# Kernel tuning notes

Hardware: AMD Instinct MI355X
Metric: run time of the kernel (lower is better)

The kernel has to match this reference:

```python
import jax, jax.numpy as jnp
import numpy as np

B, T, IN_DIM, LATENT, NUM_TOKENS = 8, 2048, 1024, 256, 4096


def setup_inputs() -> dict:
    key = jax.random.key(0)
    k1, k2, k3 = jax.random.split(key, 3)
    x = jax.random.normal(k1, (B, T, IN_DIM), dtype=jnp.float32)
    # Linear projection params (Kaiming-ish scale)
    W = jax.random.normal(k2, (IN_DIM, LATENT), dtype=jnp.float32) / np.sqrt(IN_DIM)
    b = jnp.zeros((LATENT,), dtype=jnp.float32)
    # Codebook (nn.Embedding with xavier_uniform init ~ small normal here)
    codebook = jax.random.normal(k3, (NUM_TOKENS, LATENT), dtype=jnp.float32) * 0.05
    return {"x": x, "W": W, "b": b, "codebook": codebook}


def reference(x, W, b, codebook):
    # normalization='none' -> identity; projection: Linear(in_dim, latent_dim)
    h = jnp.einsum("btd,de->bte", x, W) + b              # [B,T,latent]
    flat = h.reshape(-1, h.shape[-1])                     # [N,latent]
    # cdist + argmin: squared distance gives identical argmin as euclidean
    # d2[n,k] = |flat[n]|^2 - 2 flat@cb^T + |cb[k]|^2
    d2 = (jnp.sum(flat * flat, axis=-1, keepdims=True)
          - 2.0 * (flat @ codebook.T)
          + jnp.sum(codebook * codebook, axis=-1))        # [N,num_tokens]
    indices = jnp.argmin(d2, axis=-1)                     # [N]
    codes = codebook[indices].reshape(h.shape)            # gather -> [B,T,latent]
    idx = indices.reshape(x.shape[:-1] + (1,))            # [B,T,1]
    return codes, idx
```

## Files before the change

kernel.cpp:

```cpp
#include <hip/hip_runtime.h>

#define NROWS   16384
#define INDIM   1024
#define KDIM    256
#define NCODES  4096
#define G_ROWS  32
#define V_ROWS  64
#define NSTEP   128

#define VBUF    32768

#define MG_ROWS 64
#define MG_KC   64
#define MG_NCH  (INDIM / MG_KC)
#define XP(p)   ((p) * 8192)
#define WP(p)   (24576 + (p) * 32768)
#define MG_LDS  122880

typedef float f32x4 __attribute__((ext_vector_type(4)));
typedef int   i32x4 __attribute__((ext_vector_type(4)));
typedef short short8 __attribute__((ext_vector_type(8)));
typedef unsigned short u16x8 __attribute__((ext_vector_type(8)));
typedef unsigned short u16x4 __attribute__((ext_vector_type(4)));

__device__ inline unsigned short f2bf(float f) {
    unsigned u = __builtin_bit_cast(unsigned, f);
    u = (u + 0x7fffu + ((u >> 16) & 1u)) >> 16;
    return (unsigned short)u;
}
__device__ inline float bf2f(unsigned short h) {
    unsigned u = ((unsigned)h) << 16;
    return __builtin_bit_cast(float, u);
}
__device__ inline f32x4 mfma16(u16x8 a, u16x8 b, f32x4 c) {
    return __builtin_amdgcn_mfma_f32_16x16x32_bf16(
        __builtin_bit_cast(short8, a), __builtin_bit_cast(short8, b), c, 0, 0, 0);
}

__global__ __launch_bounds__(256) void wprep_kernel(const float* __restrict__ W,
                                                    unsigned short* __restrict__ wt_hi,
                                                    unsigned short* __restrict__ wt_md,
                                                    unsigned short* __restrict__ wt_lo) {
    const int t = threadIdx.x;
    const int k = blockIdx.x * 4 + (t >> 6);
    const int c0 = (t & 63) * 4;
    f32x4 v = *(const f32x4*)(W + (size_t)k * KDIM + c0);
    #pragma unroll
    for (int i = 0; i < 4; ++i) {
        const unsigned short h = f2bf(v[i]);
        const float r1 = v[i] - bf2f(h);
        const unsigned short m = f2bf(r1);
        const unsigned short lo = f2bf(r1 - bf2f(m));
        wt_hi[(size_t)(c0 + i) * INDIM + k] = h;
        wt_md[(size_t)(c0 + i) * INDIM + k] = m;
        wt_lo[(size_t)(c0 + i) * INDIM + k] = lo;
    }
}

__global__ __launch_bounds__(256, 1) void gemm_mfma_kernel(const float* __restrict__ x,
                                                           const unsigned short* __restrict__ wt_hi,
                                                           const unsigned short* __restrict__ wt_md,
                                                           const unsigned short* __restrict__ wt_lo,
                                                           const float* __restrict__ bvec,
                                                           float* __restrict__ hbuf) {
    __shared__ __align__(16) char lds[MG_LDS];

    const int t  = threadIdx.x;
    const int w  = t >> 6;
    const int l  = t & 63;
    const int nl = l & 15;
    const int g  = l >> 4;
    const size_t n0 = (size_t)blockIdx.x * MG_ROWS;
    const int lb = l * 16;

    f32x4 acc[4][4];
    #pragma unroll
    for (int a = 0; a < 4; ++a)
        #pragma unroll
        for (int b = 0; b < 4; ++b) acc[a][b] = (f32x4){0.f, 0.f, 0.f, 0.f};

    for (int kc = 0; kc < MG_NCH; ++kc) {
        f32x4 xa[2], xb[2];
        #pragma unroll
        for (int c = 0; c < 2; ++c) {
            const int idx = w * 2 + c;
            const int sX = idx >> 2, rsX = idx & 3;
            const float* p = x + (n0 + rsX * 16 + nl) * INDIM + kc * MG_KC + sX * 32 + g * 8;
            xa[c] = *(const f32x4*)(p);
            xb[c] = *(const f32x4*)(p + 4);
        }
        u16x8 wh[8], wm[8], wl[8];
        #pragma unroll
        for (int ci = 0; ci < 4; ++ci)
            #pragma unroll
            for (int sW = 0; sW < 2; ++sW) {
                const int q = ci * 2 + sW;
                const size_t off = (size_t)((w * 4 + ci) * 16 + nl) * INDIM
                                 + kc * MG_KC + sW * 32 + g * 8;
                wh[q] = *(const u16x8*)(wt_hi + off);
                wm[q] = *(const u16x8*)(wt_md + off);
                wl[q] = *(const u16x8*)(wt_lo + off);
            }
        __syncthreads();

        #pragma unroll
        for (int c = 0; c < 2; ++c) {
            const int idx = w * 2 + c;
            const int sX = idx >> 2, rsX = idx & 3;
            u16x8 xh, xm, xl;
            #pragma unroll
            for (int e = 0; e < 4; ++e) {
                const float a0 = xa[c][e], a1 = xb[c][e];
                const unsigned short h0 = f2bf(a0);
                const float r10 = a0 - bf2f(h0);
                const unsigned short m0 = f2bf(r10);
                const unsigned short l0 = f2bf(r10 - bf2f(m0));
                const unsigned short h1 = f2bf(a1);
                const float r11 = a1 - bf2f(h1);
                const unsigned short m1 = f2bf(r11);
                const unsigned short l1 = f2bf(r11 - bf2f(m1));
                xh[e] = h0; xh[4+e] = h1;
                xm[e] = m0; xm[4+e] = m1;
                xl[e] = l0; xl[4+e] = l1;
            }
            const int base = (sX * 4 + rsX) * 1024 + lb;
            *(u16x8*)(lds + XP(0) + base) = xh;
            *(u16x8*)(lds + XP(1) + base) = xm;
            *(u16x8*)(lds + XP(2) + base) = xl;
        }
        #pragma unroll
        for (int ci = 0; ci < 4; ++ci)
            #pragma unroll
            for (int sW = 0; sW < 2; ++sW) {
                const int q = ci * 2 + sW;
                const int base = (sW * 16 + w * 4 + ci) * 1024 + lb;
                *(u16x8*)(lds + WP(0) + base) = wh[q];
                *(u16x8*)(lds + WP(1) + base) = wm[q];
                *(u16x8*)(lds + WP(2) + base) = wl[q];
            }
        __syncthreads();

        #pragma unroll
        for (int s = 0; s < 2; ++s) {
            u16x8 bh[4], bm[4], bl[4], ah[4], am[4], al[4];
            #pragma unroll
            for (int rs = 0; rs < 4; ++rs) {
                const int base = (s * 4 + rs) * 1024 + lb;
                bh[rs] = *(const u16x8*)(lds + XP(0) + base);
                bm[rs] = *(const u16x8*)(lds + XP(1) + base);
                bl[rs] = *(const u16x8*)(lds + XP(2) + base);
            }
            #pragma unroll
            for (int ct = 0; ct < 4; ++ct) {
                const int base = (s * 16 + w * 4 + ct) * 1024 + lb;
                ah[ct] = *(const u16x8*)(lds + WP(0) + base);
                am[ct] = *(const u16x8*)(lds + WP(1) + base);
                al[ct] = *(const u16x8*)(lds + WP(2) + base);
            }
            #pragma unroll
            for (int ct = 0; ct < 4; ++ct)
                #pragma unroll
                for (int rs = 0; rs < 4; ++rs) {
                    acc[ct][rs] = mfma16(ah[ct], bh[rs], acc[ct][rs]);
                    acc[ct][rs] = mfma16(ah[ct], bm[rs], acc[ct][rs]);
                    acc[ct][rs] = mfma16(am[ct], bh[rs], acc[ct][rs]);
                    acc[ct][rs] = mfma16(ah[ct], bl[rs], acc[ct][rs]);
                    acc[ct][rs] = mfma16(al[ct], bh[rs], acc[ct][rs]);
                    acc[ct][rs] = mfma16(am[ct], bm[rs], acc[ct][rs]);
                }
        }
    }

    #pragma unroll
    for (int ct = 0; ct < 4; ++ct) {
        float bv[4];
        #pragma unroll
        for (int r = 0; r < 4; ++r) bv[r] = bvec[w * 64 + ct * 16 + g * 4 + r];
        #pragma unroll
        for (int rs = 0; rs < 4; ++rs) {
            const size_t row = n0 + rs * 16 + nl;
            #pragma unroll
            for (int r = 0; r < 4; ++r)
                hbuf[row * KDIM + w * 64 + ct * 16 + g * 4 + r] = acc[ct][rs][r] + bv[r];
        }
    }
}

__global__ __launch_bounds__(256, 2) void gemm_fb_kernel(const float* __restrict__ x,
                                                         const float* __restrict__ W,
                                                         const float* __restrict__ bvec,
                                                         float* __restrict__ hbuf) {
    const int t  = threadIdx.x;
    const int cg = t & 15;
    const int rg = t >> 4;
    const size_t n0 = (size_t)blockIdx.x * G_ROWS;
    const int c0 = cg * 16;

    float acc[2][16];
    #pragma unroll
    for (int j = 0; j < 2; ++j)
        #pragma unroll
        for (int cc = 0; cc < 16; ++cc) acc[j][cc] = 0.f;

    for (int k4 = 0; k4 < INDIM / 4; ++k4) {
        const int k = k4 * 4;
        f32x4 xv[2];
        #pragma unroll
        for (int j = 0; j < 2; ++j)
            xv[j] = *(const f32x4*)(x + (n0 + rg + 16 * j) * INDIM + k);
        f32x4 wv[4][4];
        #pragma unroll
        for (int kk = 0; kk < 4; ++kk)
            #pragma unroll
            for (int q = 0; q < 4; ++q)
                wv[kk][q] = *(const f32x4*)(W + (size_t)(k + kk) * KDIM + c0 + 4 * q);
        #pragma unroll
        for (int j = 0; j < 2; ++j)
            #pragma unroll
            for (int kk = 0; kk < 4; ++kk) {
                const float xs = xv[j][kk];
                #pragma unroll
                for (int q = 0; q < 4; ++q)
                    #pragma unroll
                    for (int e = 0; e < 4; ++e)
                        acc[j][4*q+e] = fmaf(xs, wv[kk][q][e], acc[j][4*q+e]);
            }
    }
    #pragma unroll
    for (int j = 0; j < 2; ++j) {
        float* dst = hbuf + (n0 + rg + 16 * j) * KDIM + c0;
        #pragma unroll
        for (int q = 0; q < 4; ++q) {
            f32x4 v;
            #pragma unroll
            for (int e = 0; e < 4; ++e) v[e] = acc[j][4*q+e] + bvec[c0 + 4*q + e];
            *(f32x4*)(dst + 4*q) = v;
        }
    }
}

__global__ __launch_bounds__(256) void prep_kernel(const float* __restrict__ cb,
                                                   float* __restrict__ cnorm,
                                                   unsigned short* __restrict__ cb_hi,
                                                   unsigned short* __restrict__ cb_lo,
                                                   int do_split) {
    const int c    = blockIdx.x * 4 + (threadIdx.x >> 6);
    const int lane = threadIdx.x & 63;
    f32x4 v = ((const f32x4*)(cb + (size_t)c * KDIM))[lane];
    if (do_split) {
        u16x4 h4, l4;
        #pragma unroll
        for (int j = 0; j < 4; ++j) {
            unsigned short h = f2bf(v[j]);
            h4[j] = h;
            l4[j] = f2bf(v[j] - bf2f(h));
        }
        *(u16x4*)(cb_hi + (size_t)c * KDIM + lane * 4) = h4;
        *(u16x4*)(cb_lo + (size_t)c * KDIM + lane * 4) = l4;
    }
    float s = v[0]*v[0] + v[1]*v[1] + v[2]*v[2] + v[3]*v[3];
    #pragma unroll
    for (int off = 1; off < 64; off <<= 1) s += __shfl_xor(s, off);
    if (lane == 0) cnorm[c] = s;
}

template<int PRE>
__global__ __launch_bounds__(256) void vq_partial_kernel(
    const float* __restrict__ hbuf,
    const float* __restrict__ cb,
    const float* __restrict__ cnorm,
    const unsigned short* __restrict__ cb_hi,
    const unsigned short* __restrict__ cb_lo,
    int* __restrict__ recs)
{
    __shared__ __align__(16) char lds[2 * VBUF];

    const int t  = threadIdx.x;
    const int w  = t >> 6;
    const int l  = t & 63;
    const int nl = l & 15;
    const int g  = l >> 4;
    const int lb = l * 16;
    const int bid  = blockIdx.x;
    const int half = bid & 1;
    const int S0   = half * 64;
    const size_t n0 = (size_t)(bid >> 1) * V_ROWS;
    const int row = w * 16 + nl;
    const float* hrow = hbuf + (n0 + row) * KDIM;

    u16x8 bhi[8], bmid[8];
    #pragma unroll
    for (int s = 0; s < 8; ++s) {
        f32x4 a = *(const f32x4*)(hrow + s * 32 + g * 8);
        f32x4 b = *(const f32x4*)(hrow + s * 32 + g * 8 + 4);
        u16x8 uh, um;
        #pragma unroll
        for (int jj = 0; jj < 4; ++jj) {
            unsigned short h0 = f2bf(a[jj]); uh[jj]   = h0; um[jj]   = f2bf(a[jj] - bf2f(h0));
            unsigned short h1 = f2bf(b[jj]); uh[4+jj] = h1; um[4+jj] = f2bf(b[jj] - bf2f(h1));
        }
        bhi[s] = uh; bmid[s] = um;
    }

    float v1 = 3.4e38f, v2 = 3.4e38f;
    int   i1 = 0, i2 = 0;

    u16x8 rh[2][2], rl[2][2];

    #pragma unroll
    for (int t2 = 0; t2 < 2; ++t2)
        #pragma unroll
        for (int sv = 0; sv < 2; ++sv) {
            const int sst = w * 2 + sv;
            const int code = S0 * 32 + t2 * 16 + nl;
            if (PRE) {
                const size_t off = (size_t)code * KDIM + (sst * 4 + g) * 8;
                rh[t2][sv] = *(const u16x8*)(cb_hi + off);
                rl[t2][sv] = *(const u16x8*)(cb_lo + off);
            } else {
                const float* p = cb + (size_t)code * KDIM + (sst * 4 + g) * 8;
                f32x4 a = *(const f32x4*)(p);
                f32x4 b = *(const f32x4*)(p + 4);
                u16x8 uh, ul;
                #pragma unroll
                for (int jj = 0; jj < 4; ++jj) {
                    unsigned short h0 = f2bf(a[jj]); uh[jj]   = h0; ul[jj]   = f2bf(a[jj] - bf2f(h0));
                    unsigned short h1 = f2bf(b[jj]); uh[4+jj] = h1; ul[4+jj] = f2bf(b[jj] - bf2f(h1));
                }
                rh[t2][sv] = uh; rl[t2][sv] = ul;
            }
        }
    #pragma unroll
    for (int t2 = 0; t2 < 2; ++t2)
        #pragma unroll
        for (int sv = 0; sv < 2; ++sv) {
            const int base = (t2 * 8 + w * 2 + sv) * 1024 + lb;
            *(u16x8*)(lds + base) = rh[t2][sv];
            *(u16x8*)(lds + 16384 + base) = rl[t2][sv];
        }
    __syncthreads();

    for (int S = S0; S < S0 + 64; ++S) {
        const int b = S & 1;
        if (S + 1 < S0 + 64) {
            #pragma unroll
            for (int t2 = 0; t2 < 2; ++t2)
                #pragma unroll
                for (int sv = 0; sv < 2; ++sv) {
                    const int sst = w * 2 + sv;
                    const int code = (S + 1) * 32 + t2 * 16 + nl;
                    if (PRE) {
                        const size_t off = (size_t)code * KDIM + (sst * 4 + g) * 8;
                        rh[t2][sv] = *(const u16x8*)(cb_hi + off);
                        rl[t2][sv] = *(const u16x8*)(cb_lo + off);
                    } else {
                        const float* p = cb + (size_t)code * KDIM + (sst * 4 + g) * 8;
                        f32x4 a = *(const f32x4*)(p);
                        f32x4 bb = *(const f32x4*)(p + 4);
                        u16x8 uh, ul;
                        #pragma unroll
                        for (int jj = 0; jj < 4; ++jj) {
                            unsigned short h0 = f2bf(a[jj]);  uh[jj]   = h0; ul[jj]   = f2bf(a[jj] - bf2f(h0));
                            unsigned short h1 = f2bf(bb[jj]); uh[4+jj] = h1; ul[4+jj] = f2bf(bb[jj] - bf2f(h1));
                        }
                        rh[t2][sv] = uh; rl[t2][sv] = ul;
                    }
                }
        }
        f32x4 cn0 = *(const f32x4*)(cnorm + S * 32 + g * 4);
        f32x4 cn1 = *(const f32x4*)(cnorm + S * 32 + 16 + g * 4);
        {
            const char* buf = lds + b * VBUF;
            #pragma unroll
            for (int t2 = 0; t2 < 2; ++t2) {
                f32x4 acc = {0.f, 0.f, 0.f, 0.f};
                #pragma unroll
                for (int s = 0; s < 8; ++s) {
                    const int base = (t2 * 8 + s) * 1024 + lb;
                    u16x8 ahi = *(const u16x8*)(buf + base);
                    u16x8 alo = *(const u16x8*)(buf + 16384 + base);
                    acc = mfma16(ahi, bhi[s],  acc);
                    acc = mfma16(ahi, bmid[s], acc);
                    acc = mfma16(alo, bhi[s],  acc);
                }
                const f32x4 cn = t2 ? cn1 : cn0;
                #pragma unroll
                for (int r = 0; r < 4; ++r) {
                    const float d2 = cn[r] - 2.0f * acc[r];
                    const int c = S * 32 + t2 * 16 + g * 4 + r;
                    if (d2 < v1)      { v2 = v1; i2 = i1; v1 = d2; i1 = c; }
                    else if (d2 < v2) { v2 = d2; i2 = c; }
                }
            }
        }
        __syncthreads();
        if (S + 1 < S0 + 64) {
            char* nbuf = lds + (b ^ 1) * VBUF;
            #pragma unroll
            for (int t2 = 0; t2 < 2; ++t2)
                #pragma unroll
                for (int sv = 0; sv < 2; ++sv) {
                    const int base = (t2 * 8 + w * 2 + sv) * 1024 + lb;
                    *(u16x8*)(nbuf + base) = rh[t2][sv];
                    *(u16x8*)(nbuf + 16384 + base) = rl[t2][sv];
                }
        }
        __syncthreads();
    }

    #pragma unroll
    for (int off = 16; off <= 32; off <<= 1) {
        float ov1 = __shfl_xor(v1, off); int oi1 = __shfl_xor(i1, off);
        float ov2 = __shfl_xor(v2, off); int oi2 = __shfl_xor(i2, off);
        if (ov1 < v1 || (ov1 == v1 && oi1 < i1)) {
            float tv = v1; int ti = i1; v1 = ov1; i1 = oi1; ov1 = tv; oi1 = ti;
            tv = v2; ti = i2; v2 = ov2; i2 = oi2; ov2 = tv; oi2 = ti;
        }
        if (ov1 < v2 || (ov1 == v2 && oi1 < i2)) { v2 = ov1; i2 = oi1; }
    }

    if (g == 0) {
        i32x4 rec;
        rec[0] = __builtin_bit_cast(int, v1); rec[1] = i1;
        rec[2] = __builtin_bit_cast(int, v2); rec[3] = i2;
        *(i32x4*)(recs + (((n0 + row) * 2) + half) * 4) = rec;
    }
}

__global__ __launch_bounds__(256) void vq_merge_kernel(
    float* __restrict__ hbuf,
    const float* __restrict__ cb,
    const float* __restrict__ cnorm,
    const int* __restrict__ recs,
    float* __restrict__ idx_out)
{
    const int t  = threadIdx.x;
    const int w  = t >> 6;
    const int l  = t & 63;
    const int nl = l & 15;
    const int g  = l >> 4;
    const size_t n0 = (size_t)blockIdx.x * V_ROWS;
    const int row = w * 16 + nl;
    float* hrow = hbuf + (n0 + row) * KDIM;

    const size_t rb = ((n0 + row) * 2) * 4;
    i32x4 r0 = *(const i32x4*)(recs + rb);
    i32x4 r1 = *(const i32x4*)(recs + rb + 4);
    float v1 = __builtin_bit_cast(float, r0[0]); int i1 = r0[1];
    float v2 = __builtin_bit_cast(float, r0[2]); int i2 = r0[3];
    {
        float ov1 = __builtin_bit_cast(float, r1[0]); int oi1 = r1[1];
        float ov2 = __builtin_bit_cast(float, r1[2]); int oi2 = r1[3];
        if (ov1 < v1 || (ov1 == v1 && oi1 < i1)) {
            float tv = v1; int ti = i1; v1 = ov1; i1 = oi1; ov1 = tv; oi1 = ti;
            tv = v2; ti = i2; v2 = ov2; i2 = oi2; ov2 = tv; oi2 = ti;
        }
        if (ov1 < v2 || (ov1 == v2 && oi1 < i2)) { v2 = ov1; i2 = oi1; }
    }

    i1 = (i1 < 0) ? 0 : (i1 > NCODES - 1 ? NCODES - 1 : i1);
    i2 = (i2 < 0) ? 0 : (i2 > NCODES - 1 ? NCODES - 1 : i2);

    const float* cp1 = cb + (size_t)i1 * KDIM;
    const float* cp2 = cb + (size_t)i2 * KDIM;
    float da = 0.f, db = 0.f;
    #pragma unroll
    for (int s = 0; s < 8; ++s) {
        f32x4 h0 = *(const f32x4*)(hrow + s * 32 + g * 8);
        f32x4 h1 = *(const f32x4*)(hrow + s * 32 + g * 8 + 4);
        f32x4 a1 = *(const f32x4*)(cp1 + s * 32 + g * 8);
        f32x4 b1 = *(const f32x4*)(cp1 + s * 32 + g * 8 + 4);
        f32x4 a2 = *(const f32x4*)(cp2 + s * 32 + g * 8);
        f32x4 b2 = *(const f32x4*)(cp2 + s * 32 + g * 8 + 4);
        #pragma unroll
        for (int jj = 0; jj < 4; ++jj) {
            da = fmaf(a1[jj], h0[jj], da); da = fmaf(b1[jj], h1[jj], da);
            db = fmaf(a2[jj], h0[jj], db); db = fmaf(b2[jj], h1[jj], db);
        }
    }
    da += __shfl_xor(da, 16); da += __shfl_xor(da, 32);
    db += __shfl_xor(db, 16); db += __shfl_xor(db, 32);
    const float d2a = cnorm[i1] - 2.f * da;
    const float d2b = cnorm[i2] - 2.f * db;
    const int win = (d2a < d2b || (d2a == d2b && i1 < i2)) ? i1 : i2;

    const float* cw = cb + (size_t)win * KDIM;
    #pragma unroll
    for (int s = 0; s < 8; ++s) {
        *(f32x4*)(hrow + s * 32 + g * 8)     = *(const f32x4*)(cw + s * 32 + g * 8);
        *(f32x4*)(hrow + s * 32 + g * 8 + 4) = *(const f32x4*)(cw + s * 32 + g * 8 + 4);
    }
    if (g == 0) idx_out[n0 + row] = (float)win;
}

template<int PRE>
__global__ __launch_bounds__(256) void vq_kernel(
    float* __restrict__ hbuf,
    const float* __restrict__ cb,
    const float* __restrict__ cnorm,
    const unsigned short* __restrict__ cb_hi,
    const unsigned short* __restrict__ cb_lo,
    float* __restrict__ idx_out)
{
    __shared__ __align__(16) char lds[2 * VBUF];

    const int t  = threadIdx.x;
    const int w  = t >> 6;
    const int l  = t & 63;
    const int nl = l & 15;
    const int g  = l >> 4;
    const int lb = l * 16;
    const size_t n0 = (size_t)blockIdx.x * V_ROWS;
    const int row = w * 16 + nl;
    float* hrow = hbuf + (n0 + row) * KDIM;

    u16x8 bhi[8], bmid[8];
    #pragma unroll
    for (int s = 0; s < 8; ++s) {
        f32x4 a = *(const f32x4*)(hrow + s * 32 + g * 8);
        f32x4 b = *(const f32x4*)(hrow + s * 32 + g * 8 + 4);
        u16x8 uh, um;
        #pragma unroll
        for (int jj = 0; jj < 4; ++jj) {
            unsigned short h0 = f2bf(a[jj]); uh[jj]   = h0; um[jj]   = f2bf(a[jj] - bf2f(h0));
            unsigned short h1 = f2bf(b[jj]); uh[4+jj] = h1; um[4+jj] = f2bf(b[jj] - bf2f(h1));
        }
        bhi[s] = uh; bmid[s] = um;
    }

    float v1 = 3.4e38f, v2 = 3.4e38f;
    int   i1 = 0, i2 = 0;

    u16x8 rh[2][2], rl[2][2];

    #pragma unroll
    for (int t2 = 0; t2 < 2; ++t2)
        #pragma unroll
        for (int sv = 0; sv < 2; ++sv) {
            const int sst = w * 2 + sv;
            if (PRE) {
                const size_t off = (size_t)(t2 * 16 + nl) * KDIM + (sst * 4 + g) * 8;
                rh[t2][sv] = *(const u16x8*)(cb_hi + off);
                rl[t2][sv] = *(const u16x8*)(cb_lo + off);
            } else {
                const float* p = cb + (size_t)(t2 * 16 + nl) * KDIM + (sst * 4 + g) * 8;
                f32x4 a = *(const f32x4*)(p);
                f32x4 b = *(const f32x4*)(p + 4);
                u16x8 uh, ul;
                #pragma unroll
                for (int jj = 0; jj < 4; ++jj) {
                    unsigned short h0 = f2bf(a[jj]); uh[jj]   = h0; ul[jj]   = f2bf(a[jj] - bf2f(h0));
                    unsigned short h1 = f2bf(b[jj]); uh[4+jj] = h1; ul[4+jj] = f2bf(b[jj] - bf2f(h1));
                }
                rh[t2][sv] = uh; rl[t2][sv] = ul;
            }
        }
    #pragma unroll
    for (int t2 = 0; t2 < 2; ++t2)
        #pragma unroll
        for (int sv = 0; sv < 2; ++sv) {
            const int base = (t2 * 8 + w * 2 + sv) * 1024 + lb;
            *(u16x8*)(lds + base) = rh[t2][sv];
            *(u16x8*)(lds + 16384 + base) = rl[t2][sv];
        }
    __syncthreads();

    for (int S = 0; S < NSTEP; ++S) {
        const int b = S & 1;
        if (S + 1 < NSTEP) {
            #pragma unroll
            for (int t2 = 0; t2 < 2; ++t2)
                #pragma unroll
                for (int sv = 0; sv < 2; ++sv) {
                    const int sst = w * 2 + sv;
                    const int code = (S + 1) * 32 + t2 * 16 + nl;
                    if (PRE) {
                        const size_t off = (size_t)code * KDIM + (sst * 4 + g) * 8;
                        rh[t2][sv] = *(const u16x8*)(cb_hi + off);
                        rl[t2][sv] = *(const u16x8*)(cb_lo + off);
                    } else {
                        const float* p = cb + (size_t)code * KDIM + (sst * 4 + g) * 8;
                        f32x4 a = *(const f32x4*)(p);
                        f32x4 bb = *(const f32x4*)(p + 4);
                        u16x8 uh, ul;
                        #pragma unroll
                        for (int jj = 0; jj < 4; ++jj) {
                            unsigned short h0 = f2bf(a[jj]);  uh[jj]   = h0; ul[jj]   = f2bf(a[jj] - bf2f(h0));
                            unsigned short h1 = f2bf(bb[jj]); uh[4+jj] = h1; ul[4+jj] = f2bf(bb[jj] - bf2f(h1));
                        }
                        rh[t2][sv] = uh; rl[t2][sv] = ul;
                    }
                }
        }
        f32x4 cn0 = *(const f32x4*)(cnorm + S * 32 + g * 4);
        f32x4 cn1 = *(const f32x4*)(cnorm + S * 32 + 16 + g * 4);
        {
            const char* buf = lds + b * VBUF;
            #pragma unroll
            for (int t2 = 0; t2 < 2; ++t2) {
                f32x4 acc = {0.f, 0.f, 0.f, 0.f};
                #pragma unroll
                for (int s = 0; s < 8; ++s) {
                    const int base = (t2 * 8 + s) * 1024 + lb;
                    u16x8 ahi = *(const u16x8*)(buf + base);
                    u16x8 alo = *(const u16x8*)(buf + 16384 + base);
                    acc = mfma16(ahi, bhi[s],  acc);
                    acc = mfma16(ahi, bmid[s], acc);
                    acc = mfma16(alo, bhi[s],  acc);
                }
                const f32x4 cn = t2 ? cn1 : cn0;
                #pragma unroll
                for (int r = 0; r < 4; ++r) {
                    const float d2 = cn[r] - 2.0f * acc[r];
                    const int c = S * 32 + t2 * 16 + g * 4 + r;
                    if (d2 < v1)      { v2 = v1; i2 = i1; v1 = d2; i1 = c; }
                    else if (d2 < v2) { v2 = d2; i2 = c; }
                }
            }
        }
        __syncthreads();
        if (S + 1 < NSTEP) {
            char* nbuf = lds + (b ^ 1) * VBUF;
            #pragma unroll
            for (int t2 = 0; t2 < 2; ++t2)
                #pragma unroll
                for (int sv = 0; sv < 2; ++sv) {
                    const int base = (t2 * 8 + w * 2 + sv) * 1024 + lb;
                    *(u16x8*)(nbuf + base) = rh[t2][sv];
                    *(u16x8*)(nbuf + 16384 + base) = rl[t2][sv];
                }
        }
        __syncthreads();
    }

    #pragma unroll
    for (int off = 16; off <= 32; off <<= 1) {
        float ov1 = __shfl_xor(v1, off); int oi1 = __shfl_xor(i1, off);
        float ov2 = __shfl_xor(v2, off); int oi2 = __shfl_xor(i2, off);
        if (ov1 < v1 || (ov1 == v1 && oi1 < i1)) {
            float tv = v1; int ti = i1; v1 = ov1; i1 = oi1; ov1 = tv; oi1 = ti;
            tv = v2; ti = i2; v2 = ov2; i2 = oi2; ov2 = tv; oi2 = ti;
        }
        if (ov1 < v2 || (ov1 == v2 && oi1 < i2)) { v2 = ov1; i2 = oi1; }
    }

    i1 = (i1 < 0) ? 0 : (i1 > NCODES - 1 ? NCODES - 1 : i1);
    i2 = (i2 < 0) ? 0 : (i2 > NCODES - 1 ? NCODES - 1 : i2);

    const float* cp1 = cb + (size_t)i1 * KDIM;
    const float* cp2 = cb + (size_t)i2 * KDIM;
    float da = 0.f, db = 0.f;
    #pragma unroll
    for (int s = 0; s < 8; ++s) {
        f32x4 h0 = *(const f32x4*)(hrow + s * 32 + g * 8);
        f32x4 h1 = *(const f32x4*)(hrow + s * 32 + g * 8 + 4);
        f32x4 a1 = *(const f32x4*)(cp1 + s * 32 + g * 8);
        f32x4 b1 = *(const f32x4*)(cp1 + s * 32 + g * 8 + 4);
        f32x4 a2 = *(const f32x4*)(cp2 + s * 32 + g * 8);
        f32x4 b2 = *(const f32x4*)(cp2 + s * 32 + g * 8 + 4);
        #pragma unroll
        for (int jj = 0; jj < 4; ++jj) {
            da = fmaf(a1[jj], h0[jj], da); da = fmaf(b1[jj], h1[jj], da);
            db = fmaf(a2[jj], h0[jj], db); db = fmaf(b2[jj], h1[jj], db);
        }
    }
    da += __shfl_xor(da, 16); da += __shfl_xor(da, 32);
    db += __shfl_xor(db, 16); db += __shfl_xor(db, 32);
    const float d2a = cnorm[i1] - 2.f * da;
    const float d2b = cnorm[i2] - 2.f * db;
    const int win = (d2a < d2b || (d2a == d2b && i1 < i2)) ? i1 : i2;

    const float* cw = cb + (size_t)win * KDIM;
    #pragma unroll
    for (int s = 0; s < 8; ++s) {
        *(f32x4*)(hrow + s * 32 + g * 8)     = *(const f32x4*)(cw + s * 32 + g * 8);
        *(f32x4*)(hrow + s * 32 + g * 8 + 4) = *(const f32x4*)(cw + s * 32 + g * 8 + 4);
    }
    if (g == 0) idx_out[n0 + row] = (float)win;
}

extern "C" void kernel_launch(void* const* d_in, const int* in_sizes, int n_in,
                              void* d_out, int out_size, void* d_ws, size_t ws_size,
                              hipStream_t stream) {
    (void)in_sizes; (void)n_in; (void)out_size;
    const float* x    = (const float*)d_in[0];
    const float* W    = (const float*)d_in[1];
    const float* bvec = (const float*)d_in[2];
    const float* cb   = (const float*)d_in[3];

    float* codes_out = (float*)d_out;
    float* idx_out   = (float*)d_out + (size_t)NROWS * KDIM;

    float* cnorm = (float*)d_ws;
    int*   recs  = (int*)((char*)d_ws + 16384);
    unsigned short* cb_hi = (unsigned short*)((char*)d_ws + 16384 + 524288);
    unsigned short* cb_lo = cb_hi + (size_t)NCODES * KDIM;
    unsigned short* wt_hi = cb_lo + (size_t)NCODES * KDIM;
    unsigned short* wt_md = wt_hi + (size_t)INDIM * KDIM;
    unsigned short* wt_lo = wt_md + (size_t)INDIM * KDIM;

    const size_t need_rec  = 16384 + 524288;
    const size_t need_cb   = need_rec + (size_t)NCODES * KDIM * 2 * sizeof(unsigned short);
    const size_t need_full = need_cb + (size_t)INDIM * KDIM * 3 * sizeof(unsigned short);

    const int use_split = (ws_size >= need_rec) ? 1 : 0;
    const int pre_cb    = (ws_size >= need_cb) ? 1 : 0;
    const int fast_g    = (ws_size >= need_full) ? 1 : 0;

    if (fast_g) {
        wprep_kernel<<<INDIM / 4, 256, 0, stream>>>(W, wt_hi, wt_md, wt_lo);
        gemm_mfma_kernel<<<NROWS / MG_ROWS, 256, 0, stream>>>(x, wt_hi, wt_md, wt_lo, bvec, codes_out);
    } else {
        gemm_fb_kernel<<<NROWS / G_ROWS, 256, 0, stream>>>(x, W, bvec, codes_out);
    }
    prep_kernel<<<NCODES / 4, 256, 0, stream>>>(cb, cnorm, cb_hi, cb_lo, pre_cb);

    if (use_split) {
        if (pre_cb)
            vq_partial_kernel<1><<<(NROWS / V_ROWS) * 2, 256, 0, stream>>>(codes_out, cb, cnorm, cb_hi, cb_lo, recs);
        else
            vq_partial_kernel<0><<<(NROWS / V_ROWS) * 2, 256, 0, stream>>>(codes_out, cb, cnorm, cb_hi, cb_lo, recs);
        vq_merge_kernel<<<NROWS / V_ROWS, 256, 0, stream>>>(codes_out, cb, cnorm, recs, idx_out);
    } else {
        if (pre_cb)
            vq_kernel<1><<<NROWS / V_ROWS, 256, 0, stream>>>(codes_out, cb, cnorm, cb_hi, cb_lo, idx_out);
        else
            vq_kernel<0><<<NROWS / V_ROWS, 256, 0, stream>>>(codes_out, cb, cnorm, cb_hi, cb_lo, idx_out);
    }
}
```

Measured before the change: 255.2 us.

## Split VQ search into quarters with 128-row tiles and 8-candidate exact rescoring

The partial VQ kernel now gives each block 128 rows (two 16-row sets per wave) and a quarter of the codebook, so each codebook tile staged in LDS feeds twice as many MFMAs. Each block stores only its top-2 indices per quarter, and the merge kernel rescores all 8 candidates exactly in fp32. The aim is to cut LDS and codebook traffic per unit of MFMA work while keeping the block count. In exchange it raises register pressure (launch bounds set to 2 blocks per CU) and adds more fp32 rescoring work in the merge.

```diff
diff --git a/kernel.cpp b/kernel.cpp
--- a/kernel.cpp
+++ b/kernel.cpp
@@ -6,6 +6,7 @@
 #define NCODES  4096
 #define G_ROWS  32
 #define V_ROWS  64
+#define P_ROWS  128
 #define NSTEP   128
 
 #define VBUF    32768
@@ -18,7 +19,7 @@
 #define MG_LDS  122880
 
 typedef float f32x4 __attribute__((ext_vector_type(4)));
-typedef int   i32x4 __attribute__((ext_vector_type(4)));
+typedef int   i32x2 __attribute__((ext_vector_type(2)));
 typedef short short8 __attribute__((ext_vector_type(8)));
 typedef unsigned short u16x8 __attribute__((ext_vector_type(8)));
 typedef unsigned short u16x4 __attribute__((ext_vector_type(4)));
@@ -265,7 +266,7 @@
 }
 
 template<int PRE>
-__global__ __launch_bounds__(256) void vq_partial_kernel(
+__global__ __launch_bounds__(256, 2) void vq_partial_kernel(
     const float* __restrict__ hbuf,
     const float* __restrict__ cb,
     const float* __restrict__ cnorm,
@@ -282,28 +283,30 @@
     const int g  = l >> 4;
     const int lb = l * 16;
     const int bid  = blockIdx.x;
-    const int half = bid & 1;
-    const int S0   = half * 64;
-    const size_t n0 = (size_t)(bid >> 1) * V_ROWS;
-    const int row = w * 16 + nl;
-    const float* hrow = hbuf + (n0 + row) * KDIM;
-
-    u16x8 bhi[8], bmid[8];
-    #pragma unroll
-    for (int s = 0; s < 8; ++s) {
-        f32x4 a = *(const f32x4*)(hrow + s * 32 + g * 8);
-        f32x4 b = *(const f32x4*)(hrow + s * 32 + g * 8 + 4);
-        u16x8 uh, um;
-        #pragma unroll
-        for (int jj = 0; jj < 4; ++jj) {
-            unsigned short h0 = f2bf(a[jj]); uh[jj]   = h0; um[jj]   = f2bf(a[jj] - bf2f(h0));
-            unsigned short h1 = f2bf(b[jj]); uh[4+jj] = h1; um[4+jj] = f2bf(b[jj] - bf2f(h1));
-        }
-        bhi[s] = uh; bmid[s] = um;
-    }
-
-    float v1 = 3.4e38f, v2 = 3.4e38f;
-    int   i1 = 0, i2 = 0;
+    const int quar = bid & 3;
+    const int S0   = quar * 32;
+    const size_t n0 = (size_t)(bid >> 2) * P_ROWS;
+
+    u16x8 bhi[2][8], bmid[2][8];
+    #pragma unroll
+    for (int rset = 0; rset < 2; ++rset) {
+        const float* hrow = hbuf + (n0 + w * 32 + rset * 16 + nl) * KDIM;
+        #pragma unroll
+        for (int s = 0; s < 8; ++s) {
+            f32x4 a = *(const f32x4*)(hrow + s * 32 + g * 8);
+            f32x4 b = *(const f32x4*)(hrow + s * 32 + g * 8 + 4);
+            u16x8 uh, um;
+            #pragma unroll
+            for (int jj = 0; jj < 4; ++jj) {
+                unsigned short h0 = f2bf(a[jj]); uh[jj]   = h0; um[jj]   = f2bf(a[jj] - bf2f(h0));
+                unsigned short h1 = f2bf(b[jj]); uh[4+jj] = h1; um[4+jj] = f2bf(b[jj] - bf2f(h1));
+            }
+            bhi[rset][s] = uh; bmid[rset][s] = um;
+        }
+    }
+
+    float v1[2] = {3.4e38f, 3.4e38f}, v2[2] = {3.4e38f, 3.4e38f};
+    int   i1[2] = {0, 0},            i2[2] = {0, 0};
 
     u16x8 rh[2][2], rl[2][2];
 
@@ -340,9 +343,9 @@
         }
     __syncthreads();
 
-    for (int S = S0; S < S0 + 64; ++S) {
+    for (int S = S0; S < S0 + 32; ++S) {
         const int b = S & 1;
-        if (S + 1 < S0 + 64) {
+        if (S + 1 < S0 + 32) {
             #pragma unroll
             for (int t2 = 0; t2 < 2; ++t2)
                 #pragma unroll
@@ -373,28 +376,35 @@
             const char* buf = lds + b * VBUF;
             #pragma unroll
             for (int t2 = 0; t2 < 2; ++t2) {
-                f32x4 acc = {0.f, 0.f, 0.f, 0.f};
+                f32x4 acc0 = {0.f, 0.f, 0.f, 0.f};
+                f32x4 acc1 = {0.f, 0.f, 0.f, 0.f};
                 #pragma unroll
                 for (int s = 0; s < 8; ++s) {
                     const int base = (t2 * 8 + s) * 1024 + lb;
                     u16x8 ahi = *(const u16x8*)(buf + base);
                     u16x8 alo = *(const u16x8*)(buf + 16384 + base);
-                    acc = mfma16(ahi, bhi[s],  acc);
-                    acc = mfma16(ahi, bmid[s], acc);
-                    acc = mfma16(alo, bhi[s],  acc);
+                    acc0 = mfma16(ahi, bhi[0][s],  acc0);
+                    acc0 = mfma16(ahi, bmid[0][s], acc0);
+                    acc0 = mfma16(alo, bhi[0][s],  acc0);
+                    acc1 = mfma16(ahi, bhi[1][s],  acc1);
+                    acc1 = mfma16(ahi, bmid[1][s], acc1);
+                    acc1 = mfma16(alo, bhi[1][s],  acc1);
                 }
                 const f32x4 cn = t2 ? cn1 : cn0;
                 #pragma unroll
                 for (int r = 0; r < 4; ++r) {
-                    const float d2 = cn[r] - 2.0f * acc[r];
                     const int c = S * 32 + t2 * 16 + g * 4 + r;
-                    if (d2 < v1)      { v2 = v1; i2 = i1; v1 = d2; i1 = c; }
-                    else if (d2 < v2) { v2 = d2; i2 = c; }
+                    const float d0 = cn[r] - 2.0f * acc0[r];
+                    if (d0 < v1[0])      { v2[0] = v1[0]; i2[0] = i1[0]; v1[0] = d0; i1[0] = c; }
+                    else if (d0 < v2[0]) { v2[0] = d0; i2[0] = c; }
+                    const float d1 = cn[r] - 2.0f * acc1[r];
+                    if (d1 < v1[1])      { v2[1] = v1[1]; i2[1] = i1[1]; v1[1] = d1; i1[1] = c; }
+                    else if (d1 < v2[1]) { v2[1] = d1; i2[1] = c; }
                 }
             }
         }
         __syncthreads();
-        if (S + 1 < S0 + 64) {
+        if (S + 1 < S0 + 32) {
             char* nbuf = lds + (b ^ 1) * VBUF;
             #pragma unroll
             for (int t2 = 0; t2 < 2; ++t2)
@@ -409,21 +419,27 @@
     }
 
     #pragma unroll
-    for (int off = 16; off <= 32; off <<= 1) {
-        float ov1 = __shfl_xor(v1, off); int oi1 = __shfl_xor(i1, off);
-        float ov2 = __shfl_xor(v2, off); int oi2 = __shfl_xor(i2, off);
-        if (ov1 < v1 || (ov1 == v1 && oi1 < i1)) {
-            float tv = v1; int ti = i1; v1 = ov1; i1 = oi1; ov1 = tv; oi1 = ti;
-            tv = v2; ti = i2; v2 = ov2; i2 = oi2; ov2 = tv; oi2 = ti;
-        }
-        if (ov1 < v2 || (ov1 == v2 && oi1 < i2)) { v2 = ov1; i2 = oi1; }
+    for (int rset = 0; rset < 2; ++rset) {
+        #pragma unroll
+        for (int off = 16; off <= 32; off <<= 1) {
+            float ov1 = __shfl_xor(v1[rset], off); int oi1 = __shfl_xor(i1[rset], off);
+            float ov2 = __shfl_xor(v2[rset], off); int oi2 = __shfl_xor(i2[rset], off);
+            if (ov1 < v1[rset] || (ov1 == v1[rset] && oi1 < i1[rset])) {
+                float tv = v1[rset]; int ti = i1[rset]; v1[rset] = ov1; i1[rset] = oi1; ov1 = tv; oi1 = ti;
+                tv = v2[rset]; ti = i2[rset]; v2[rset] = ov2; i2[rset] = oi2; ov2 = tv; oi2 = ti;
+            }
+            if (ov1 < v2[rset] || (ov1 == v2[rset] && oi1 < i2[rset])) { v2[rset] = ov1; i2[rset] = oi1; }
+        }
     }
 
     if (g == 0) {
-        i32x4 rec;
-        rec[0] = __builtin_bit_cast(int, v1); rec[1] = i1;
-        rec[2] = __builtin_bit_cast(int, v2); rec[3] = i2;
-        *(i32x4*)(recs + (((n0 + row) * 2) + half) * 4) = rec;
+        #pragma unroll
+        for (int rset = 0; rset < 2; ++rset) {
+            i32x2 rec;
+            rec[0] = i1[rset]; rec[1] = i2[rset];
+            const size_t row = n0 + w * 32 + rset * 16 + nl;
+            *(i32x2*)(recs + (row * 4 + quar) * 2) = rec;
+        }
     }
 }
 
@@ -443,54 +459,54 @@
     const int row = w * 16 + nl;
     float* hrow = hbuf + (n0 + row) * KDIM;
 
-    const size_t rb = ((n0 + row) * 2) * 4;
-    i32x4 r0 = *(const i32x4*)(recs + rb);
-    i32x4 r1 = *(const i32x4*)(recs + rb + 4);
-    float v1 = __builtin_bit_cast(float, r0[0]); int i1 = r0[1];
-    float v2 = __builtin_bit_cast(float, r0[2]); int i2 = r0[3];
+    int cand[8];
     {
-        float ov1 = __builtin_bit_cast(float, r1[0]); int oi1 = r1[1];
-        float ov2 = __builtin_bit_cast(float, r1[2]); int oi2 = r1[3];
-        if (ov1 < v1 || (ov1 == v1 && oi1 < i1)) {
-            float tv = v1; int ti = i1; v1 = ov1; i1 = oi1; ov1 = tv; oi1 = ti;
-            tv = v2; ti = i2; v2 = ov2; i2 = oi2; ov2 = tv; oi2 = ti;
-        }
-        if (ov1 < v2 || (ov1 == v2 && oi1 < i2)) { v2 = ov1; i2 = oi1; }
-    }
-
-    i1 = (i1 < 0) ? 0 : (i1 > NCODES - 1 ? NCODES - 1 : i1);
-    i2 = (i2 < 0) ? 0 : (i2 > NCODES - 1 ? NCODES - 1 : i2);
-
-    const float* cp1 = cb + (size_t)i1 * KDIM;
-    const float* cp2 = cb + (size_t)i2 * KDIM;
-    float da = 0.f, db = 0.f;
+        const size_t rb = (n0 + row) * 8;
+        #pragma unroll
+        for (int q = 0; q < 4; ++q) {
+            i32x2 rq = *(const i32x2*)(recs + rb + q * 2);
+            int a = rq[0], b = rq[1];
+            cand[2*q]   = (a < 0) ? 0 : (a > NCODES - 1 ? NCODES - 1 : a);
+            cand[2*q+1] = (b < 0) ? 0 : (b > NCODES - 1 ? NCODES - 1 : b);
+        }
+    }
+
+    f32x4 hreg[16];
     #pragma unroll
     for (int s = 0; s < 8; ++s) {
-        f32x4 h0 = *(const f32x4*)(hrow + s * 32 + g * 8);
-        f32x4 h1 = *(const f32x4*)(hrow + s * 32 + g * 8 + 4);
-        f32x4 a1 = *(const f32x4*)(cp1 + s * 32 + g * 8);
-        f32x4 b1 = *(const f32x4*)(cp1 + s * 32 + g * 8 + 4);
-        f32x4 a2 = *(const f32x4*)(cp2 + s * 32 + g * 8);
-        f32x4 b2 = *(const f32x4*)(cp2 + s * 32 + g * 8 + 4);
-        #pragma unroll
-        for (int jj = 0; jj < 4; ++jj) {
-            da = fmaf(a1[jj], h0[jj], da); da = fmaf(b1[jj], h1[jj], da);
-            db = fmaf(a2[jj], h0[jj], db); db = fmaf(b2[jj], h1[jj], db);
-        }
-    }
-    da += __shfl_xor(da, 16); da += __shfl_xor(da, 32);
-    db += __shfl_xor(db, 16); db += __shfl_xor(db, 32);
-    const float d2a = cnorm[i1] - 2.f * da;
-    const float d2b = cnorm[i2] - 2.f * db;
-    const int win = (d2a < d2b || (d2a == d2b && i1 < i2)) ? i1 : i2;
-
-    const float* cw = cb + (size_t)win * KDIM;
+        hreg[2*s]   = *(const f32x4*)(hrow + s * 32 + g * 8);
+        hreg[2*s+1] = *(const f32x4*)(hrow + s * 32 + g * 8 + 4);
+    }
+
+    float bestd = 3.4e38f;
+    int   besti = 0x7fffffff;
+    #pragma unroll
+    for (int k = 0; k < 8; ++k) {
+        const int ci = cand[k];
+        const float* cp = cb + (size_t)ci * KDIM;
+        float d = 0.f;
+        #pragma unroll
+        for (int s = 0; s < 8; ++s) {
+            f32x4 a = *(const f32x4*)(cp + s * 32 + g * 8);
+            f32x4 b = *(const f32x4*)(cp + s * 32 + g * 8 + 4);
+            #pragma unroll
+            for (int jj = 0; jj < 4; ++jj) {
+                d = fmaf(a[jj], hreg[2*s][jj], d);
+                d = fmaf(b[jj], hreg[2*s+1][jj], d);
+            }
+        }
+        d += __shfl_xor(d, 16); d += __shfl_xor(d, 32);
+        const float d2 = cnorm[ci] - 2.f * d;
+        if (d2 < bestd || (d2 == bestd && ci < besti)) { bestd = d2; besti = ci; }
+    }
+
+    const float* cw = cb + (size_t)besti * KDIM;
     #pragma unroll
     for (int s = 0; s < 8; ++s) {
         *(f32x4*)(hrow + s * 32 + g * 8)     = *(const f32x4*)(cw + s * 32 + g * 8);
         *(f32x4*)(hrow + s * 32 + g * 8 + 4) = *(const f32x4*)(cw + s * 32 + g * 8 + 4);
     }
-    if (g == 0) idx_out[n0 + row] = (float)win;
+    if (g == 0) idx_out[n0 + row] = (float)besti;
 }
 
 template<int PRE>
@@ -717,9 +733,9 @@
 
     if (use_split) {
         if (pre_cb)
-            vq_partial_kernel<1><<<(NROWS / V_ROWS) * 2, 256, 0, stream>>>(codes_out, cb, cnorm, cb_hi, cb_lo, recs);
+            vq_partial_kernel<1><<<(NROWS / P_ROWS) * 4, 256, 0, stream>>>(codes_out, cb, cnorm, cb_hi, cb_lo, recs);
         else
-            vq_partial_kernel<0><<<(NROWS / V_ROWS) * 2, 256, 0, stream>>>(codes_out, cb, cnorm, cb_hi, cb_lo, recs);
+            vq_partial_kernel<0><<<(NROWS / P_ROWS) * 4, 256, 0, stream>>>(codes_out, cb, cnorm, cb_hi, cb_lo, recs);
         vq_merge_kernel<<<NROWS / V_ROWS, 256, 0, stream>>>(codes_out, cb, cnorm, recs, idx_out);
     } else {
         if (pre_cb)
```

Result: slower. 262.3 us (+2.8%).
